# Performance work log

Measured on AMD Instinct MI355X. Metric: run time of the kernel, lower is better.

Reference implementation:

```python
import jax, jax.numpy as jnp
import numpy as np

N = 36          # number of independent LSTM streams (input_dim)
H = 256         # hidden units
G = 4 * H       # gate width (i, f, g, o)
SPEC = 6
OUT = 30
B, T = 32, 128


def setup_inputs() -> dict:
    key = jax.random.key(0)
    ks = jax.random.split(key, 18)
    s = 0.05
    d = {}
    d["x"] = jax.random.normal(ks[0], (B, T, N), dtype=jnp.float32)
    d["spec"] = jax.random.normal(ks[1], (B, SPEC), dtype=jnp.float32)
    # 36 stacked 2-layer LSTMs, batched along leading stream axis N.
    # Layer 1: input_size=1, so W_ih collapses to [N, G].
    d["Wih1"] = jax.random.normal(ks[2], (N, G), dtype=jnp.float32) * s
    d["Whh1"] = jax.random.normal(ks[3], (N, G, H), dtype=jnp.float32) * s
    d["bih1"] = jax.random.normal(ks[4], (N, G), dtype=jnp.float32) * s
    d["bhh1"] = jax.random.normal(ks[5], (N, G), dtype=jnp.float32) * s
    # Layer 2: input_size=H.
    d["Wih2"] = jax.random.normal(ks[6], (N, G, H), dtype=jnp.float32) * s
    d["Whh2"] = jax.random.normal(ks[7], (N, G, H), dtype=jnp.float32) * s
    d["bih2"] = jax.random.normal(ks[8], (N, G), dtype=jnp.float32) * s
    d["bhh2"] = jax.random.normal(ks[9], (N, G), dtype=jnp.float32) * s
    # spec_dense: Linear(6, H); stored as [in, out].
    d["Wspec"] = jax.random.normal(ks[10], (SPEC, H), dtype=jnp.float32) * s
    d["bspec"] = jax.random.normal(ks[11], (H,), dtype=jnp.float32) * s
    # predicter: Linear(H*(N+1), H) -> ReLU -> Linear(H, OUT); stored as [in, out].
    d["Wp1"] = jax.random.normal(ks[12], (H * (N + 1), H), dtype=jnp.float32) * s
    d["bp1"] = jax.random.normal(ks[13], (H,), dtype=jnp.float32) * s
    d["Wp2"] = jax.random.normal(ks[14], (H, OUT), dtype=jnp.float32) * s
    d["bp2"] = jax.random.normal(ks[15], (OUT,), dtype=jnp.float32) * s
    return d


def _lstm_cell(gates, c):
    # torch gate order: input, forget, cell(g), output
    i, f, g, o = jnp.split(gates, 4, axis=-1)
    c = jax.nn.sigmoid(f) * c + jax.nn.sigmoid(i) * jnp.tanh(g)
    h = jax.nn.sigmoid(o) * jnp.tanh(c)
    return h, c


def reference(x, spec, Wih1, Whh1, bih1, bhh1, Wih2, Whh2, bih2, bhh2,
              Wspec, bspec, Wp1, bp1, Wp2, bp2):
    b = x.shape[0]
    bg1 = bih1 + bhh1  # [N, G]
    bg2 = bih2 + bhh2

    def step(carry, x_t):
        # x_t: [B, N] scalar input per stream at this timestep
        h1, c1, h2, c2 = carry
        g1 = x_t[:, :, None] * Wih1[None] + jnp.einsum('bnh,ngh->bng', h1, Whh1) + bg1
        h1, c1 = _lstm_cell(g1, c1)
        g2 = (jnp.einsum('bnh,ngh->bng', h1, Wih2)
              + jnp.einsum('bnh,ngh->bng', h2, Whh2) + bg2)
        h2, c2 = _lstm_cell(g2, c2)
        return (h1, c1, h2, c2), None

    z = jnp.zeros((b, N, H), x.dtype)
    (h1, c1, h2, c2), _ = jax.lax.scan(step, (z, z, z, z), jnp.transpose(x, (1, 0, 2)))
    hidden_all = h2.reshape(b, N * H)          # concat of last-step top-layer h per stream
    hidden_spec = spec @ Wspec + bspec         # [B, H]
    feat = jnp.concatenate([hidden_all, hidden_spec], axis=1)  # [B, (N+1)*H]
    return jax.nn.relu(feat @ Wp1 + bp1) @ Wp2 + bp2
```

## Files before the change

### kernel.cpp

```cpp
#include <hip/hip_runtime.h>
#include <cstdint>
#include <cstddef>


constexpr int kN = 36, kH = 256, kG = 1024, kB = 32, kT = 128, kSpec = 6, kOut = 30;
constexpr int kHP = 264;
constexpr int kD1 = 16;

typedef __bf16 bf16;
typedef __bf16 bf16x8 __attribute__((ext_vector_type(8)));
typedef float f32x4 __attribute__((ext_vector_type(4)));
typedef unsigned long long u64;
typedef unsigned int u32;

__device__ __forceinline__ float rcpf(float v) { return __builtin_amdgcn_rcpf(v); }
__device__ __forceinline__ float sigm(float v) { return rcpf(1.f + __expf(-v)); }
__device__ __forceinline__ float tanh_f(float v) {
  return fmaf(-2.f, rcpf(1.f + __expf(2.f * v)), 1.f);
}
__device__ __forceinline__ unsigned short f2bf(float f) {
  bf16 b = (bf16)f;
  return __builtin_bit_cast(unsigned short, b);
}
__device__ __forceinline__ u64 pload(const u64* p) {
  return __hip_atomic_load(p, __ATOMIC_RELAXED, __HIP_MEMORY_SCOPE_AGENT);
}
__device__ __forceinline__ void pstore(u64* p, u64 v) {
  __hip_atomic_store(p, v, __ATOMIC_RELAXED, __HIP_MEMORY_SCOPE_AGENT);
}
__device__ __forceinline__ u32 pload32(const u32* p) {
  return __hip_atomic_load(p, __ATOMIC_RELAXED, __HIP_MEMORY_SCOPE_AGENT);
}
__device__ __forceinline__ void pstore32(u32* p, u32 v) {
  __hip_atomic_store(p, v, __ATOMIC_RELAXED, __HIP_MEMORY_SCOPE_AGENT);
}


__device__ __forceinline__ void issue16(const u64* __restrict__ base, int tid, u64* v) {
#pragma unroll
  for (int i = 0; i < 16; ++i) v[i] = pload(base + (size_t)i * 256 + tid);
}
__device__ __forceinline__ void finish16(const u64* __restrict__ base, u32 want,
                                         int tid, u64* v) {
  u32 got = 0;
  for (;;) {
#pragma unroll
    for (int i = 0; i < 16; ++i)
      if (!(got & (1u << i)) && (u32)(v[i] >> 32) == want) got |= 1u << i;
    if (got == 0xFFFFu) return;
#pragma unroll
    for (int i = 0; i < 16; ++i)
      if (!(got & (1u << i))) v[i] = pload(base + (size_t)i * 256 + tid);
  }
}
__device__ __forceinline__ void finish16_stage(const u64* __restrict__ base, u32 want,
                                               int tid, unsigned short (*hs)[kHP],
                                               u64* v) {
  u32 got = 0;
  for (;;) {
#pragma unroll
    for (int i = 0; i < 16; ++i) {
      if (!(got & (1u << i)) && (u32)(v[i] >> 32) == want) {
        got |= 1u << i;
        hs[i][tid] = (unsigned short)v[i];
        hs[i + 16][tid] = (unsigned short)(v[i] >> 16);
      }
    }
    if (got == 0xFFFFu) return;
#pragma unroll
    for (int i = 0; i < 16; ++i)
      if (!(got & (1u << i))) v[i] = pload(base + (size_t)i * 256 + tid);
  }
}
__device__ __forceinline__ void issue8h(const u64* __restrict__ base, int tid, int pc0,
                                        u64* v) {
  const int c = pc0 + (tid & 127), m0 = (tid >> 7) * 8;
#pragma unroll
  for (int i = 0; i < 8; ++i) v[i] = pload(base + (size_t)(m0 + i) * 256 + c);
}
__device__ __forceinline__ void finish8_stage(const u64* __restrict__ base, u32 want,
                                              int tid, int pc0,
                                              unsigned short (*hs)[kHP], u64* v) {
  const int c = pc0 + (tid & 127), m0 = (tid >> 7) * 8;
  u32 got = 0;
  for (;;) {
#pragma unroll
    for (int i = 0; i < 8; ++i) {
      if (!(got & (1u << i)) && (u32)(v[i] >> 32) == want) {
        got |= 1u << i;
        hs[m0 + i][c] = (unsigned short)v[i];
        hs[m0 + i + 16][c] = (unsigned short)(v[i] >> 16);
      }
    }
    if (got == 0xFFu) return;
#pragma unroll
    for (int i = 0; i < 8; ++i)
      if (!(got & (1u << i))) v[i] = pload(base + (size_t)(m0 + i) * 256 + c);
  }
}

__global__ __launch_bounds__(256) void k_convert(
    const float* __restrict__ wa, const float* __restrict__ wb, const float* __restrict__ wc,
    bf16* __restrict__ oa, bf16* __restrict__ ob, bf16* __restrict__ oc)
{
  const size_t total = (size_t)kN * 64 * 8 * 64;
  size_t gid = (size_t)blockIdx.x * 256 + threadIdx.x;
  if (gid >= total) return;
  const int lane = (int)(gid & 63);
  const int ks = (int)((gid >> 6) & 7);
  const int nt = (int)((gid >> 9) & 63);
  const int n = (int)(gid >> 15);
  const int g = nt * 16 + (lane & 15);
  const int k = ks * 32 + (lane >> 4) * 8;
  const size_t so = ((size_t)n * kG + g) * kH + k;

  const float4 a0 = *(const float4*)(wa + so), a1 = *(const float4*)(wa + so + 4);
  const float4 b0 = *(const float4*)(wb + so), b1 = *(const float4*)(wb + so + 4);
  const float4 c0 = *(const float4*)(wc + so), c1 = *(const float4*)(wc + so + 4);
  bf16x8 va, vb, vc;
  va[0]=(bf16)a0.x; va[1]=(bf16)a0.y; va[2]=(bf16)a0.z; va[3]=(bf16)a0.w;
  va[4]=(bf16)a1.x; va[5]=(bf16)a1.y; va[6]=(bf16)a1.z; va[7]=(bf16)a1.w;
  vb[0]=(bf16)b0.x; vb[1]=(bf16)b0.y; vb[2]=(bf16)b0.z; vb[3]=(bf16)b0.w;
  vb[4]=(bf16)b1.x; vb[5]=(bf16)b1.y; vb[6]=(bf16)b1.z; vb[7]=(bf16)b1.w;
  vc[0]=(bf16)c0.x; vc[1]=(bf16)c0.y; vc[2]=(bf16)c0.z; vc[3]=(bf16)c0.w;
  vc[4]=(bf16)c1.x; vc[5]=(bf16)c1.y; vc[6]=(bf16)c1.z; vc[7]=(bf16)c1.w;
  ((bf16x8*)oa)[gid] = va;
  ((bf16x8*)ob)[gid] = vb;
  ((bf16x8*)oc)[gid] = vc;
}

#define L1_MFMA_HALF(KS0)                                                            \
  _Pragma("unroll")                                                                  \
  for (int kk = 0; kk < 4; ++kk) {                                                   \
    const int ks = (KS0) + kk;                                                       \
    bf16x8 A0 = *(const bf16x8*)&hs1[l15][ks * 32 + l4 * 8];                         \
    bf16x8 A1 = *(const bf16x8*)&hs1[16 + l15][ks * 32 + l4 * 8];                    \
    _Pragma("unroll")                                                                \
    for (int jj = 0; jj < 2; ++jj)                                                   \
      _Pragma("unroll")                                                              \
      for (int gt = 0; gt < 4; ++gt) {                                               \
        acc[0][jj][gt] = __builtin_amdgcn_mfma_f32_16x16x32_bf16(                    \
            A0, W[jj][gt][ks], acc[0][jj][gt], 0, 0, 0);                             \
        acc[1][jj][gt] = __builtin_amdgcn_mfma_f32_16x16x32_bf16(                    \
            A1, W[jj][gt][ks], acc[1][jj][gt], 0, 0, 0);                             \
      }                                                                              \
  }

__global__ __launch_bounds__(256) __attribute__((amdgpu_waves_per_eu(1, 1)))
void k_lstm(
    const float* __restrict__ x, const float* __restrict__ Wih1,
    const float* __restrict__ bih1, const float* __restrict__ bhh1,
    const float* __restrict__ bih2, const float* __restrict__ bhh2,
    const bf16* __restrict__ pk1, const bf16* __restrict__ pk2i,
    const bf16* __restrict__ pk2h, float* __restrict__ h2_final,
    u64* __restrict__ h1r, u64* __restrict__ h2r, u32* __restrict__ prog)
{
  const int blk = blockIdx.x;
  const int tid = threadIdx.x, wv = tid >> 6, lane = tid & 63;
  const int l15 = lane & 15, l4 = lane >> 4;

  __shared__ alignas(16) unsigned short hs1[kB][kHP];

  if (blk < 72) {
    const int n = blk >> 1, j = blk & 1;
    __shared__ float xsh[kT][kB];
    for (int i = tid; i < kB * kT; i += 256) {
      int b = i >> 7, t = i & 127;
      xsh[t][b] = x[((size_t)b * kT + t) * kN + n];
    }
    bf16x8 W[2][4][8];
    {
      const bf16x8* base = (const bf16x8*)pk1 + (size_t)n * 32768;
#pragma unroll
      for (int jj = 0; jj < 2; ++jj)
#pragma unroll
        for (int gt = 0; gt < 4; ++gt)
#pragma unroll
          for (int ks = 0; ks < 8; ++ks)
            W[jj][gt][ks] = base[(size_t)(gt * 16 + j * 8 + wv * 2 + jj) * 512 + ks * 64 + lane];
    }
    float wih[2][4], bg[2][4];
#pragma unroll
    for (int jj = 0; jj < 2; ++jj)
#pragma unroll
      for (int gt = 0; gt < 4; ++gt) {
        int g = gt * 256 + j * 128 + wv * 32 + jj * 16 + l15;
        wih[jj][gt] = Wih1[n * kG + g];
        bg[jj][gt] = bih1[n * kG + g] + bhh1[n * kG + g];
      }
    float cst[2][2][4];
#pragma unroll
    for (int a = 0; a < 2; ++a)
#pragma unroll
      for (int b = 0; b < 2; ++b)
#pragma unroll
        for (int r = 0; r < 4; ++r) cst[a][b][r] = 0.f;

    u64* ringn = h1r + (size_t)n * kD1 * 4096;
    u32* pg = prog + n * 4;
    const int pc0 = (1 - j) * 128, myb = j * 128 + wv * 32;
    u64 pv[8];
    __syncthreads();

#pragma unroll 1
    for (int t = 0; t < kT; ++t) {
      if ((t & 7) == 0 && t) {
        if (tid == 0) {
          for (;;) {
            u32 m0 = pload32(&pg[0]), m1 = pload32(&pg[1]);
            u32 m2 = pload32(&pg[2]), m3 = pload32(&pg[3]);
            u32 mn = m0 < m1 ? m0 : m1;
            mn = mn < m2 ? mn : m2;
            mn = mn < m3 ? mn : m3;
            if ((int)mn + 8 >= t) break;
          }
        }
        __syncthreads();
      }
      f32x4 acc[2][2][4];
#pragma unroll
      for (int mt = 0; mt < 2; ++mt)
#pragma unroll
        for (int jj = 0; jj < 2; ++jj)
#pragma unroll
          for (int gt = 0; gt < 4; ++gt)
#pragma unroll
            for (int r = 0; r < 4; ++r)
              acc[mt][jj][gt][r] = xsh[t][mt * 16 + l4 * 4 + r] * wih[jj][gt] + bg[jj][gt];
      if (t > 0) {
        const u64* ps = ringn + (size_t)((t - 1) % kD1) * 4096;
        if (j == 0) { L1_MFMA_HALF(0) } else { L1_MFMA_HALF(4) }
        finish8_stage(ps, (u32)t, tid, pc0, hs1, pv);
        __syncthreads();
        if (j == 0) { L1_MFMA_HALF(4) } else { L1_MFMA_HALF(0) }
      }
      u64* pub = ringn + (size_t)(t % kD1) * 4096;
      const u64 tagw = ((u64)(u32)(t + 1)) << 32;
      float hv[2][2][4];
#pragma unroll
      for (int jj = 0; jj < 2; ++jj) {
#pragma unroll
        for (int mt = 0; mt < 2; ++mt)
#pragma unroll
          for (int r = 0; r < 4; ++r) {
            float cc = sigm(acc[mt][jj][1][r]) * cst[mt][jj][r]
                     + sigm(acc[mt][jj][0][r]) * tanh_f(acc[mt][jj][2][r]);
            cst[mt][jj][r] = cc;
            hv[mt][jj][r] = sigm(acc[mt][jj][3][r]) * tanh_f(cc);
          }
#pragma unroll
        for (int r = 0; r < 4; ++r) {
          int c = myb + jj * 16 + l15, m = l4 * 4 + r;
          pstore(&pub[(size_t)m * 256 + c],
                 tagw | ((u64)f2bf(hv[1][jj][r]) << 16) | f2bf(hv[0][jj][r]));
        }
      }
#pragma unroll
      for (int mt = 0; mt < 2; ++mt)
#pragma unroll
        for (int jj = 0; jj < 2; ++jj)
#pragma unroll
          for (int r = 0; r < 4; ++r)
            hs1[mt * 16 + l4 * 4 + r][myb + jj * 16 + l15] = f2bf(hv[mt][jj][r]);
      if (t + 1 < kT) issue8h(pub, tid, pc0, pv);
      __syncthreads();
    }
  } else {
    const int bb = blk - 72, n = bb >> 2, q = bb & 3;
    __shared__ alignas(16) unsigned short hs2[kB][kHP];

    bf16x8 Wi[4][8], Wh[4][8];
    {
      const bf16x8* bi = (const bf16x8*)pk2i + (size_t)n * 32768;
      const bf16x8* bh = (const bf16x8*)pk2h + (size_t)n * 32768;
#pragma unroll
      for (int gt = 0; gt < 4; ++gt)
#pragma unroll
        for (int ks = 0; ks < 8; ++ks) {
          size_t o = (size_t)(gt * 16 + q * 4 + wv) * 512 + ks * 64 + lane;
          Wi[gt][ks] = bi[o];
          Wh[gt][ks] = bh[o];
        }
    }
    const int col = q * 64 + wv * 16 + l15;
    float bg[4];
#pragma unroll
    for (int gt = 0; gt < 4; ++gt) {
      int g = gt * 256 + col;
      bg[gt] = bih2[n * kG + g] + bhh2[n * kG + g];
    }
    float cst[2][4];
#pragma unroll
    for (int mt = 0; mt < 2; ++mt)
#pragma unroll
      for (int r = 0; r < 4; ++r) cst[mt][r] = 0.f;

    u64* ringn = h1r + (size_t)n * kD1 * 4096;
    u64* h2n = h2r + (size_t)n * 2 * 4096;
    u32* pg = prog + n * 4 + q;
    __syncthreads();

    u64 v1[16], v2[16];
    issue16(ringn, tid, v1);
    finish16(ringn, 1u, tid, v1);

#pragma unroll 1
    for (int t = 0; t < kT; ++t) {
#pragma unroll
      for (int i = 0; i < 16; ++i) {
        hs1[i][tid] = (unsigned short)v1[i];
        hs1[i + 16][tid] = (unsigned short)(v1[i] >> 16);
      }
      __syncthreads();
      if (tid == 0) pstore32(pg, (u32)(t + 1));
      const u64* pn = ringn + (size_t)((t + 1) % kD1) * 4096;
      if (t + 1 < kT) issue16(pn, tid, v1);
      f32x4 acc[2][4];
#pragma unroll
      for (int mt = 0; mt < 2; ++mt)
#pragma unroll
        for (int gt = 0; gt < 4; ++gt)
#pragma unroll
          for (int r = 0; r < 4; ++r) acc[mt][gt][r] = bg[gt];
#pragma unroll
      for (int ks = 0; ks < 8; ++ks) {
        bf16x8 A0 = *(const bf16x8*)&hs1[l15][ks * 32 + l4 * 8];
        bf16x8 A1 = *(const bf16x8*)&hs1[16 + l15][ks * 32 + l4 * 8];
#pragma unroll
        for (int gt = 0; gt < 4; ++gt) {
          acc[0][gt] = __builtin_amdgcn_mfma_f32_16x16x32_bf16(A0, Wi[gt][ks], acc[0][gt], 0, 0, 0);
          acc[1][gt] = __builtin_amdgcn_mfma_f32_16x16x32_bf16(A1, Wi[gt][ks], acc[1][gt], 0, 0, 0);
        }
      }
      if (t > 0) {
        finish16_stage(h2n + (size_t)((t - 1) & 1) * 4096, (u32)t, tid, hs2, v2);
        __syncthreads();
#pragma unroll
        for (int ks = 0; ks < 8; ++ks) {
          bf16x8 A0 = *(const bf16x8*)&hs2[l15][ks * 32 + l4 * 8];
          bf16x8 A1 = *(const bf16x8*)&hs2[16 + l15][ks * 32 + l4 * 8];
#pragma unroll
          for (int gt = 0; gt < 4; ++gt) {
            acc[0][gt] = __builtin_amdgcn_mfma_f32_16x16x32_bf16(A0, Wh[gt][ks], acc[0][gt], 0, 0, 0);
            acc[1][gt] = __builtin_amdgcn_mfma_f32_16x16x32_bf16(A1, Wh[gt][ks], acc[1][gt], 0, 0, 0);
          }
        }
      }
      u64* pub = h2n + (size_t)(t & 1) * 4096;
      const u64 tagw = ((u64)(u32)(t + 1)) << 32;
      float hv[2][4];
#pragma unroll
      for (int r = 0; r < 4; ++r) {
#pragma unroll
        for (int mt = 0; mt < 2; ++mt) {
          float cc = sigm(acc[mt][1][r]) * cst[mt][r]
                   + sigm(acc[mt][0][r]) * tanh_f(acc[mt][2][r]);
          cst[mt][r] = cc;
          hv[mt][r] = sigm(acc[mt][3][r]) * tanh_f(cc);
        }
        pstore(&pub[(size_t)(l4 * 4 + r) * 256 + col],
               tagw | ((u64)f2bf(hv[1][r]) << 16) | f2bf(hv[0][r]));
      }
      if (t == kT - 1) {
#pragma unroll
        for (int mt = 0; mt < 2; ++mt)
#pragma unroll
          for (int r = 0; r < 4; ++r)
            h2_final[((size_t)n * kB + (mt * 16 + l4 * 4 + r)) * kH + col] = hv[mt][r];
      }
      if (t + 1 < kT) issue16(pub, tid, v2);
      if (t + 1 < kT) finish16(pn, (u32)(t + 2), tid, v1);
      __syncthreads();
    }
  }
}

__global__ __launch_bounds__(256) void k_head1(
    const float* __restrict__ spec, const float* __restrict__ Wspec,
    const float* __restrict__ bspec, const float* __restrict__ Wp1,
    const float* __restrict__ h2f, float* __restrict__ partial)
{
  const int kc = blockIdx.x;
  const int b = blockIdx.y;
  const int o = threadIdx.x;
  __shared__ float fs[kH];
  if (kc < kN) {
    fs[o] = h2f[((size_t)kc * kB + b) * kH + o];
  } else {
    float v = bspec[o];
#pragma unroll
    for (int s = 0; s < kSpec; ++s) v += spec[b * kSpec + s] * Wspec[s * kH + o];
    fs[o] = v;
  }
  __syncthreads();
  const float* __restrict__ wp = Wp1 + (size_t)kc * 256 * kH + o;
  float a = 0.f;
#pragma unroll 8
  for (int i = 0; i < 256; ++i) a += fs[i] * wp[(size_t)i * kH];
  partial[((size_t)kc * kB + b) * kH + o] = a;
}

__global__ __launch_bounds__(256) void k_head2(
    const float* __restrict__ bp1, const float* __restrict__ Wp2,
    const float* __restrict__ bp2, const float* __restrict__ partial,
    float* __restrict__ out)
{
  const int b = blockIdx.x;
  const int o = threadIdx.x;
  __shared__ float hid[kH];
  float a = bp1[o];
#pragma unroll
  for (int kc = 0; kc < kN + 1; ++kc) a += partial[((size_t)kc * kB + b) * kH + o];
  hid[o] = fmaxf(a, 0.f);
  __syncthreads();
  if (o < kOut) {
    float r = bp2[o];
#pragma unroll 8
    for (int h = 0; h < kH; ++h) r += hid[h] * Wp2[h * kOut + o];
    out[b * kOut + o] = r;
  }
}

extern "C" void kernel_launch(void* const* d_in, const int* in_sizes, int n_in,
                              void* d_out, int out_size, void* d_ws, size_t ws_size,
                              hipStream_t stream) {
  const float* x = (const float*)d_in[0];
  const float* spec = (const float*)d_in[1];
  const float* Wih1 = (const float*)d_in[2];
  const float* Whh1 = (const float*)d_in[3];
  const float* bih1 = (const float*)d_in[4];
  const float* bhh1 = (const float*)d_in[5];
  const float* Wih2 = (const float*)d_in[6];
  const float* Whh2 = (const float*)d_in[7];
  const float* bih2 = (const float*)d_in[8];
  const float* bhh2 = (const float*)d_in[9];
  const float* Wspec = (const float*)d_in[10];
  const float* bspec = (const float*)d_in[11];
  const float* Wp1 = (const float*)d_in[12];
  const float* bp1 = (const float*)d_in[13];
  const float* Wp2 = (const float*)d_in[14];
  const float* bp2 = (const float*)d_in[15];
  float* out = (float*)d_out;

  const size_t WSZ = (size_t)kN * kG * kH;
  u32* prog = (u32*)d_ws;
  u64* h1r = (u64*)((char*)d_ws + 4096);
  u64* h2r = h1r + (size_t)kN * kD1 * 4096;
  bf16* pk1 = (bf16*)(h2r + (size_t)kN * 2 * 4096);
  bf16* pk2i = pk1 + WSZ;
  bf16* pk2h = pk2i + WSZ;
  float* h2_final = (float*)(pk2h + WSZ);
  float* partial = h2_final + (size_t)kN * kB * kH;

  hipMemsetAsync(d_ws, 0, 4096, stream);

  const size_t groups = (size_t)kN * 64 * 8 * 64;
  k_convert<<<dim3((unsigned)((groups + 255) / 256)), dim3(256), 0, stream>>>(
      Whh1, Wih2, Whh2, pk1, pk2i, pk2h);
  k_lstm<<<dim3(216), dim3(256), 0, stream>>>(
      x, Wih1, bih1, bhh1, bih2, bhh2, pk1, pk2i, pk2h, h2_final, h1r, h2r, prog);
  k_head1<<<dim3(kN + 1, kB), dim3(256), 0, stream>>>(spec, Wspec, bspec, Wp1, h2_final, partial);
  k_head2<<<dim3(kB), dim3(256), 0, stream>>>(bp1, Wp2, bp2, partial, out);
}
```

Baseline: 879.2 us.

## Keep own h2 slice locally and rotate K order to overlap peer waits

Each layer-2 block now writes its own freshly computed h2 columns straight into shared memory and fetches only the other three quarter-slices from peers (12 loads instead of 16). The Whh2 K-chunks are rotated so the chunks this block owns locally are multiplied first, before it waits on peer data, hiding part of the cross-block handoff latency. Staging of the next h1 into shared memory is also moved to the end of the step, which removes one barrier per step. Correctness now depends on the rotated weight indexing and the column mapping (fm/fc) matching exactly, and the per-element index arrays add register pressure.

```diff
diff --git a/kernel.cpp b/kernel.cpp
--- a/kernel.cpp
+++ b/kernel.cpp
@@ -53,23 +53,28 @@
       if (!(got & (1u << i))) v[i] = pload(base + (size_t)i * 256 + tid);
   }
 }
-__device__ __forceinline__ void finish16_stage(const u64* __restrict__ base, u32 want,
-                                               int tid, unsigned short (*hs)[kHP],
-                                               u64* v) {
+__device__ __forceinline__ void issue12(const u64* __restrict__ base, const int* fm,
+                                        const int* fc, u64* v) {
+#pragma unroll
+  for (int i = 0; i < 12; ++i) v[i] = pload(base + (size_t)fm[i] * 256 + fc[i]);
+}
+__device__ __forceinline__ void finish12_stage(const u64* __restrict__ base, u32 want,
+                                               const int* fm, const int* fc,
+                                               unsigned short (*hs)[kHP], u64* v) {
   u32 got = 0;
   for (;;) {
 #pragma unroll
-    for (int i = 0; i < 16; ++i) {
+    for (int i = 0; i < 12; ++i) {
       if (!(got & (1u << i)) && (u32)(v[i] >> 32) == want) {
         got |= 1u << i;
-        hs[i][tid] = (unsigned short)v[i];
-        hs[i + 16][tid] = (unsigned short)(v[i] >> 16);
-      }
-    }
-    if (got == 0xFFFFu) return;
-#pragma unroll
-    for (int i = 0; i < 16; ++i)
-      if (!(got & (1u << i))) v[i] = pload(base + (size_t)i * 256 + tid);
+        hs[fm[i]][fc[i]] = (unsigned short)v[i];
+        hs[fm[i] + 16][fc[i]] = (unsigned short)(v[i] >> 16);
+      }
+    }
+    if (got == 0xFFFu) return;
+#pragma unroll
+    for (int i = 0; i < 12; ++i)
+      if (!(got & (1u << i))) v[i] = pload(base + (size_t)fm[i] * 256 + fc[i]);
   }
 }
 __device__ __forceinline__ void issue8h(const u64* __restrict__ base, int tid, int pc0,
@@ -276,11 +281,22 @@
 #pragma unroll
       for (int gt = 0; gt < 4; ++gt)
 #pragma unroll
-        for (int ks = 0; ks < 8; ++ks) {
-          size_t o = (size_t)(gt * 16 + q * 4 + wv) * 512 + ks * 64 + lane;
-          Wi[gt][ks] = bi[o];
-          Wh[gt][ks] = bh[o];
-        }
+        for (int i = 0; i < 8; ++i) {
+          size_t nt = (size_t)(gt * 16 + q * 4 + wv) * 512;
+          Wi[gt][i] = bi[nt + (size_t)i * 64 + lane];
+          Wh[gt][i] = bh[nt + (size_t)((2 * q + i) & 7) * 64 + lane];
+        }
+    }
+    int cb[8];
+#pragma unroll
+    for (int i = 0; i < 8; ++i) cb[i] = ((2 * q + i) & 7) * 32;
+    int fm[12], fc[12];
+#pragma unroll
+    for (int i = 0; i < 12; ++i) {
+      int p = tid * 12 + i;
+      int m = p / 192;
+      fm[i] = m;
+      fc[i] = (q * 64 + 64 + (p - m * 192)) & 255;
     }
     const int col = q * 64 + wv * 16 + l15;
     float bg[4];
@@ -300,18 +316,18 @@
     u32* pg = prog + n * 4 + q;
     __syncthreads();
 
-    u64 v1[16], v2[16];
+    u64 v1[16], v2[12];
     issue16(ringn, tid, v1);
     finish16(ringn, 1u, tid, v1);
+#pragma unroll
+    for (int i = 0; i < 16; ++i) {
+      hs1[i][tid] = (unsigned short)v1[i];
+      hs1[i + 16][tid] = (unsigned short)(v1[i] >> 16);
+    }
+    __syncthreads();
 
 #pragma unroll 1
     for (int t = 0; t < kT; ++t) {
-#pragma unroll
-      for (int i = 0; i < 16; ++i) {
-        hs1[i][tid] = (unsigned short)v1[i];
-        hs1[i + 16][tid] = (unsigned short)(v1[i] >> 16);
-      }
-      __syncthreads();
       if (tid == 0) pstore32(pg, (u32)(t + 1));
       const u64* pn = ringn + (size_t)((t + 1) % kD1) * 4096;
       if (t + 1 < kT) issue16(pn, tid, v1);
@@ -333,18 +349,30 @@
         }
       }
       if (t > 0) {
-        finish16_stage(h2n + (size_t)((t - 1) & 1) * 4096, (u32)t, tid, hs2, v2);
+#pragma unroll
+        for (int i = 0; i < 2; ++i) {
+          bf16x8 A0 = *(const bf16x8*)&hs2[l15][cb[i] + l4 * 8];
+          bf16x8 A1 = *(const bf16x8*)&hs2[16 + l15][cb[i] + l4 * 8];
+#pragma unroll
+          for (int gt = 0; gt < 4; ++gt) {
+            acc[0][gt] = __builtin_amdgcn_mfma_f32_16x16x32_bf16(A0, Wh[gt][i], acc[0][gt], 0, 0, 0);
+            acc[1][gt] = __builtin_amdgcn_mfma_f32_16x16x32_bf16(A1, Wh[gt][i], acc[1][gt], 0, 0, 0);
+          }
+        }
+        finish12_stage(h2n + (size_t)((t - 1) & 1) * 4096, (u32)t, fm, fc, hs2, v2);
         __syncthreads();
 #pragma unroll
-        for (int ks = 0; ks < 8; ++ks) {
-          bf16x8 A0 = *(const bf16x8*)&hs2[l15][ks * 32 + l4 * 8];
-          bf16x8 A1 = *(const bf16x8*)&hs2[16 + l15][ks * 32 + l4 * 8];
+        for (int i = 2; i < 8; ++i) {
+          bf16x8 A0 = *(const bf16x8*)&hs2[l15][cb[i] + l4 * 8];
+          bf16x8 A1 = *(const bf16x8*)&hs2[16 + l15][cb[i] + l4 * 8];
 #pragma unroll
           for (int gt = 0; gt < 4; ++gt) {
-            acc[0][gt] = __builtin_amdgcn_mfma_f32_16x16x32_bf16(A0, Wh[gt][ks], acc[0][gt], 0, 0, 0);
-            acc[1][gt] = __builtin_amdgcn_mfma_f32_16x16x32_bf16(A1, Wh[gt][ks], acc[1][gt], 0, 0, 0);
+            acc[0][gt] = __builtin_amdgcn_mfma_f32_16x16x32_bf16(A0, Wh[gt][i], acc[0][gt], 0, 0, 0);
+            acc[1][gt] = __builtin_amdgcn_mfma_f32_16x16x32_bf16(A1, Wh[gt][i], acc[1][gt], 0, 0, 0);
           }
         }
+      } else {
+        __syncthreads();
       }
       u64* pub = h2n + (size_t)(t & 1) * 4096;
       const u64 tagw = ((u64)(u32)(t + 1)) << 32;
@@ -360,6 +388,8 @@
         }
         pstore(&pub[(size_t)(l4 * 4 + r) * 256 + col],
                tagw | ((u64)f2bf(hv[1][r]) << 16) | f2bf(hv[0][r]));
+        hs2[l4 * 4 + r][col] = f2bf(hv[0][r]);
+        hs2[l4 * 4 + r + 16][col] = f2bf(hv[1][r]);
       }
       if (t == kT - 1) {
 #pragma unroll
@@ -368,8 +398,15 @@
           for (int r = 0; r < 4; ++r)
             h2_final[((size_t)n * kB + (mt * 16 + l4 * 4 + r)) * kH + col] = hv[mt][r];
       }
-      if (t + 1 < kT) issue16(pub, tid, v2);
-      if (t + 1 < kT) finish16(pn, (u32)(t + 2), tid, v1);
+      if (t + 1 < kT) issue12(pub, fm, fc, v2);
+      if (t + 1 < kT) {
+        finish16(pn, (u32)(t + 2), tid, v1);
+#pragma unroll
+        for (int i = 0; i < 16; ++i) {
+          hs1[i][tid] = (unsigned short)v1[i];
+          hs1[i + 16][tid] = (unsigned short)(v1[i] >> 16);
+        }
+      }
       __syncthreads();
     }
   }
```

Result: slower. 1.878 ms (+113.6%).

## Overlap layer-2 recurrent MFMA with peer h2 exchange via rotated K order

Applied to the files above, without the earlier changes.

Each layer-2 block now writes its own freshly computed h2 slice directly into local shared memory. It also rotates the K-chunk order of the recurrent weights so the first two chunks, its own columns, are multiplied before waiting on the other blocks' published h2. This overlaps part of the recurrent GEMM with the cross-block exchange latency. The risk is a race: the local hs2 writes happen before the barrier that finish16_stage and later reads rely on, so ordering against the staged copy must stay correct.

```diff
diff --git a/kernel.cpp b/kernel.cpp
--- a/kernel.cpp
+++ b/kernel.cpp
@@ -276,12 +276,15 @@
 #pragma unroll
       for (int gt = 0; gt < 4; ++gt)
 #pragma unroll
-        for (int ks = 0; ks < 8; ++ks) {
-          size_t o = (size_t)(gt * 16 + q * 4 + wv) * 512 + ks * 64 + lane;
-          Wi[gt][ks] = bi[o];
-          Wh[gt][ks] = bh[o];
-        }
-    }
+        for (int i = 0; i < 8; ++i) {
+          size_t nt = (size_t)(gt * 16 + q * 4 + wv) * 512;
+          Wi[gt][i] = bi[nt + (size_t)i * 64 + lane];
+          Wh[gt][i] = bh[nt + (size_t)((2 * q + i) & 7) * 64 + lane];
+        }
+    }
+    int cb[8];
+#pragma unroll
+    for (int i = 0; i < 8; ++i) cb[i] = ((2 * q + i) & 7) * 32;
     const int col = q * 64 + wv * 16 + l15;
     float bg[4];
 #pragma unroll
@@ -333,16 +336,26 @@
         }
       }
       if (t > 0) {
+#pragma unroll
+        for (int i = 0; i < 2; ++i) {
+          bf16x8 A0 = *(const bf16x8*)&hs2[l15][cb[i] + l4 * 8];
+          bf16x8 A1 = *(const bf16x8*)&hs2[16 + l15][cb[i] + l4 * 8];
+#pragma unroll
+          for (int gt = 0; gt < 4; ++gt) {
+            acc[0][gt] = __builtin_amdgcn_mfma_f32_16x16x32_bf16(A0, Wh[gt][i], acc[0][gt], 0, 0, 0);
+            acc[1][gt] = __builtin_amdgcn_mfma_f32_16x16x32_bf16(A1, Wh[gt][i], acc[1][gt], 0, 0, 0);
+          }
+        }
         finish16_stage(h2n + (size_t)((t - 1) & 1) * 4096, (u32)t, tid, hs2, v2);
         __syncthreads();
 #pragma unroll
-        for (int ks = 0; ks < 8; ++ks) {
-          bf16x8 A0 = *(const bf16x8*)&hs2[l15][ks * 32 + l4 * 8];
-          bf16x8 A1 = *(const bf16x8*)&hs2[16 + l15][ks * 32 + l4 * 8];
+        for (int i = 2; i < 8; ++i) {
+          bf16x8 A0 = *(const bf16x8*)&hs2[l15][cb[i] + l4 * 8];
+          bf16x8 A1 = *(const bf16x8*)&hs2[16 + l15][cb[i] + l4 * 8];
 #pragma unroll
           for (int gt = 0; gt < 4; ++gt) {
-            acc[0][gt] = __builtin_amdgcn_mfma_f32_16x16x32_bf16(A0, Wh[gt][ks], acc[0][gt], 0, 0, 0);
-            acc[1][gt] = __builtin_amdgcn_mfma_f32_16x16x32_bf16(A1, Wh[gt][ks], acc[1][gt], 0, 0, 0);
+            acc[0][gt] = __builtin_amdgcn_mfma_f32_16x16x32_bf16(A0, Wh[gt][i], acc[0][gt], 0, 0, 0);
+            acc[1][gt] = __builtin_amdgcn_mfma_f32_16x16x32_bf16(A1, Wh[gt][i], acc[1][gt], 0, 0, 0);
           }
         }
       }
@@ -360,6 +373,8 @@
         }
         pstore(&pub[(size_t)(l4 * 4 + r) * 256 + col],
                tagw | ((u64)f2bf(hv[1][r]) << 16) | f2bf(hv[0][r]));
+        hs2[l4 * 4 + r][col] = f2bf(hv[0][r]);
+        hs2[l4 * 4 + r + 16][col] = f2bf(hv[1][r]);
       }
       if (t == kT - 1) {
 #pragma unroll
```

New measurement: 1.005 ms. 1.14x slower.

## Colocate each stream's blocks on one XCD and add fast-path h exchange

Applied to the files above, without the earlier changes.

Blocks are remapped so that all six workgroups of a stream (two layer-1, four layer-2) land on the same XCD, assuming round-robin dispatch by block index. Each producer also writes its tagged hidden-state packets to a second double-buffered array with ordinary stores. Consumers first poll that array with batched sc0 inline-asm loads, which the XCD-local L2 may serve without the system-coherent path, and fall back to the original polling after repeated misses. The goal is lower cross-block handoff latency per timestep, at the cost of extra stores, a larger workspace, 24 idle blocks, and reliance on the dispatch-order assumption and on sc0 coherence semantics.

```diff
diff --git a/kernel.cpp b/kernel.cpp
--- a/kernel.cpp
+++ b/kernel.cpp
@@ -97,6 +97,78 @@
     for (int i = 0; i < 8; ++i)
       if (!(got & (1u << i))) v[i] = pload(base + (size_t)(m0 + i) * 256 + c);
   }
+}
+
+__device__ __forceinline__ void fast_load16(const u64* fb, int tid, u64* v) {
+  const u64* b0 = fb + 2 * 256 + tid;
+  const u64* b1 = fb + 6 * 256 + tid;
+  const u64* b2 = fb + 10 * 256 + tid;
+  const u64* b3 = fb + 14 * 256 + tid;
+  asm volatile(
+      "global_load_dwordx2 %0, %16, off offset:-4096 sc0\n\t"
+      "global_load_dwordx2 %1, %16, off offset:-2048 sc0\n\t"
+      "global_load_dwordx2 %2, %16, off sc0\n\t"
+      "global_load_dwordx2 %3, %16, off offset:2048 sc0\n\t"
+      "global_load_dwordx2 %4, %17, off offset:-4096 sc0\n\t"
+      "global_load_dwordx2 %5, %17, off offset:-2048 sc0\n\t"
+      "global_load_dwordx2 %6, %17, off sc0\n\t"
+      "global_load_dwordx2 %7, %17, off offset:2048 sc0\n\t"
+      "global_load_dwordx2 %8, %18, off offset:-4096 sc0\n\t"
+      "global_load_dwordx2 %9, %18, off offset:-2048 sc0\n\t"
+      "global_load_dwordx2 %10, %18, off sc0\n\t"
+      "global_load_dwordx2 %11, %18, off offset:2048 sc0\n\t"
+      "global_load_dwordx2 %12, %19, off offset:-4096 sc0\n\t"
+      "global_load_dwordx2 %13, %19, off offset:-2048 sc0\n\t"
+      "global_load_dwordx2 %14, %19, off sc0\n\t"
+      "global_load_dwordx2 %15, %19, off offset:2048 sc0\n\t"
+      "s_waitcnt vmcnt(0)"
+      : "=v"(v[0]), "=v"(v[1]), "=v"(v[2]), "=v"(v[3]),
+        "=v"(v[4]), "=v"(v[5]), "=v"(v[6]), "=v"(v[7]),
+        "=v"(v[8]), "=v"(v[9]), "=v"(v[10]), "=v"(v[11]),
+        "=v"(v[12]), "=v"(v[13]), "=v"(v[14]), "=v"(v[15])
+      : "v"(b0), "v"(b1), "v"(b2), "v"(b3)
+      : "memory");
+}
+__device__ __forceinline__ bool fast_try16(const u64* fb, u32 want, int tid, u64* v,
+                                           int budget) {
+  for (int it = 0; it < budget; ++it) {
+    fast_load16(fb, tid, v);
+    bool all = true;
+#pragma unroll
+    for (int i = 0; i < 16; ++i) all &= ((u32)(v[i] >> 32) == want);
+    if (all) return true;
+  }
+  return false;
+}
+__device__ __forceinline__ void fast_load8(const u64* fb, int tid, int pc0, u64* v) {
+  const int c = pc0 + (tid & 127), m0 = (tid >> 7) * 8;
+  const u64* b0 = fb + (size_t)(m0 + 2) * 256 + c;
+  const u64* b1 = fb + (size_t)(m0 + 6) * 256 + c;
+  asm volatile(
+      "global_load_dwordx2 %0, %8, off offset:-4096 sc0\n\t"
+      "global_load_dwordx2 %1, %8, off offset:-2048 sc0\n\t"
+      "global_load_dwordx2 %2, %8, off sc0\n\t"
+      "global_load_dwordx2 %3, %8, off offset:2048 sc0\n\t"
+      "global_load_dwordx2 %4, %9, off offset:-4096 sc0\n\t"
+      "global_load_dwordx2 %5, %9, off offset:-2048 sc0\n\t"
+      "global_load_dwordx2 %6, %9, off sc0\n\t"
+      "global_load_dwordx2 %7, %9, off offset:2048 sc0\n\t"
+      "s_waitcnt vmcnt(0)"
+      : "=v"(v[0]), "=v"(v[1]), "=v"(v[2]), "=v"(v[3]),
+        "=v"(v[4]), "=v"(v[5]), "=v"(v[6]), "=v"(v[7])
+      : "v"(b0), "v"(b1)
+      : "memory");
+}
+__device__ __forceinline__ bool fast_try8(const u64* fb, u32 want, int tid, int pc0,
+                                          u64* v, int budget) {
+  for (int it = 0; it < budget; ++it) {
+    fast_load8(fb, tid, pc0, v);
+    bool all = true;
+#pragma unroll
+    for (int i = 0; i < 8; ++i) all &= ((u32)(v[i] >> 32) == want);
+    if (all) return true;
+  }
+  return false;
 }
 
 __global__ __launch_bounds__(256) void k_convert(
@@ -153,16 +225,21 @@
     const float* __restrict__ bih2, const float* __restrict__ bhh2,
     const bf16* __restrict__ pk1, const bf16* __restrict__ pk2i,
     const bf16* __restrict__ pk2h, float* __restrict__ h2_final,
-    u64* __restrict__ h1r, u64* __restrict__ h2r, u32* __restrict__ prog)
+    u64* __restrict__ h1r, u64* __restrict__ h2r,
+    u64* __restrict__ fh1, u64* __restrict__ fh2, u32* __restrict__ prog)
 {
   const int blk = blockIdx.x;
+  const int xcd = blk & 7, sl = blk >> 3;
+  const int kk_ = sl / 6, w = sl - kk_ * 6;
+  const int n = kk_ * 8 + xcd;
+  if (n >= kN) return;
   const int tid = threadIdx.x, wv = tid >> 6, lane = tid & 63;
   const int l15 = lane & 15, l4 = lane >> 4;
 
   __shared__ alignas(16) unsigned short hs1[kB][kHP];
 
-  if (blk < 72) {
-    const int n = blk >> 1, j = blk & 1;
+  if (w < 2) {
+    const int j = w;
     __shared__ float xsh[kT][kB];
     for (int i = tid; i < kB * kT; i += 256) {
       int b = i >> 7, t = i & 127;
@@ -197,9 +274,11 @@
         for (int r = 0; r < 4; ++r) cst[a][b][r] = 0.f;
 
     u64* ringn = h1r + (size_t)n * kD1 * 4096;
+    u64* fh1n = fh1 + (size_t)n * 2 * 4096;
     u32* pg = prog + n * 4;
     const int pc0 = (1 - j) * 128, myb = j * 128 + wv * 32;
-    u64 pv[8];
+    u64 pv[8], vf[8];
+    int fen = 1, fmiss = 0;
     __syncthreads();
 
 #pragma unroll 1
@@ -230,11 +309,25 @@
       if (t > 0) {
         const u64* ps = ringn + (size_t)((t - 1) % kD1) * 4096;
         if (j == 0) { L1_MFMA_HALF(0) } else { L1_MFMA_HALF(4) }
-        finish8_stage(ps, (u32)t, tid, pc0, hs1, pv);
+        bool fok = false;
+        if (fen) fok = fast_try8(fh1n + (size_t)((t - 1) & 1) * 4096, (u32)t, tid, pc0, vf, 12);
+        if (fok) {
+          const int c = pc0 + (tid & 127), m0 = (tid >> 7) * 8;
+          fmiss = 0;
+#pragma unroll
+          for (int i = 0; i < 8; ++i) {
+            hs1[m0 + i][c] = (unsigned short)vf[i];
+            hs1[m0 + i + 16][c] = (unsigned short)(vf[i] >> 16);
+          }
+        } else {
+          if (fen && ++fmiss >= 4) fen = 0;
+          finish8_stage(ps, (u32)t, tid, pc0, hs1, pv);
+        }
         __syncthreads();
         if (j == 0) { L1_MFMA_HALF(4) } else { L1_MFMA_HALF(0) }
       }
       u64* pub = ringn + (size_t)(t % kD1) * 4096;
+      u64* fpub = fh1n + (size_t)(t & 1) * 4096;
       const u64 tagw = ((u64)(u32)(t + 1)) << 32;
       float hv[2][2][4];
 #pragma unroll
@@ -251,8 +344,9 @@
 #pragma unroll
         for (int r = 0; r < 4; ++r) {
           int c = myb + jj * 16 + l15, m = l4 * 4 + r;
-          pstore(&pub[(size_t)m * 256 + c],
-                 tagw | ((u64)f2bf(hv[1][jj][r]) << 16) | f2bf(hv[0][jj][r]));
+          u64 pkt = tagw | ((u64)f2bf(hv[1][jj][r]) << 16) | f2bf(hv[0][jj][r]);
+          fpub[(size_t)m * 256 + c] = pkt;
+          pstore(&pub[(size_t)m * 256 + c], pkt);
         }
       }
 #pragma unroll
@@ -266,7 +360,7 @@
       __syncthreads();
     }
   } else {
-    const int bb = blk - 72, n = bb >> 2, q = bb & 3;
+    const int q = w - 2;
     __shared__ alignas(16) unsigned short hs2[kB][kHP];
 
     bf16x8 Wi[4][8], Wh[4][8];
@@ -297,10 +391,12 @@
 
     u64* ringn = h1r + (size_t)n * kD1 * 4096;
     u64* h2n = h2r + (size_t)n * 2 * 4096;
+    u64* fh2n = fh2 + (size_t)n * 2 * 4096;
     u32* pg = prog + n * 4 + q;
+    int fen = 1, fmiss = 0;
     __syncthreads();
 
-    u64 v1[16], v2[16];
+    u64 v1[16], v2[16], vf[16];
     issue16(ringn, tid, v1);
     finish16(ringn, 1u, tid, v1);
 
@@ -333,7 +429,19 @@
         }
       }
       if (t > 0) {
-        finish16_stage(h2n + (size_t)((t - 1) & 1) * 4096, (u32)t, tid, hs2, v2);
+        bool fok = false;
+        if (fen) fok = fast_try16(fh2n + (size_t)((t - 1) & 1) * 4096, (u32)t, tid, vf, 12);
+        if (fok) {
+          fmiss = 0;
+#pragma unroll
+          for (int i = 0; i < 16; ++i) {
+            hs2[i][tid] = (unsigned short)vf[i];
+            hs2[i + 16][tid] = (unsigned short)(vf[i] >> 16);
+          }
+        } else {
+          if (fen && ++fmiss >= 4) fen = 0;
+          finish16_stage(h2n + (size_t)((t - 1) & 1) * 4096, (u32)t, tid, hs2, v2);
+        }
         __syncthreads();
 #pragma unroll
         for (int ks = 0; ks < 8; ++ks) {
@@ -347,6 +455,7 @@
         }
       }
       u64* pub = h2n + (size_t)(t & 1) * 4096;
+      u64* fpub = fh2n + (size_t)(t & 1) * 4096;
       const u64 tagw = ((u64)(u32)(t + 1)) << 32;
       float hv[2][4];
 #pragma unroll
@@ -358,8 +467,9 @@
           cst[mt][r] = cc;
           hv[mt][r] = sigm(acc[mt][3][r]) * tanh_f(cc);
         }
-        pstore(&pub[(size_t)(l4 * 4 + r) * 256 + col],
-               tagw | ((u64)f2bf(hv[1][r]) << 16) | f2bf(hv[0][r]));
+        u64 pkt = tagw | ((u64)f2bf(hv[1][r]) << 16) | f2bf(hv[0][r]);
+        fpub[(size_t)(l4 * 4 + r) * 256 + col] = pkt;
+        pstore(&pub[(size_t)(l4 * 4 + r) * 256 + col], pkt);
       }
       if (t == kT - 1) {
 #pragma unroll
@@ -446,7 +556,9 @@
   u32* prog = (u32*)d_ws;
   u64* h1r = (u64*)((char*)d_ws + 4096);
   u64* h2r = h1r + (size_t)kN * kD1 * 4096;
-  bf16* pk1 = (bf16*)(h2r + (size_t)kN * 2 * 4096);
+  u64* fh1 = h2r + (size_t)kN * 2 * 4096;
+  u64* fh2 = fh1 + (size_t)kN * 2 * 4096;
+  bf16* pk1 = (bf16*)(fh2 + (size_t)kN * 2 * 4096);
   bf16* pk2i = pk1 + WSZ;
   bf16* pk2h = pk2i + WSZ;
   float* h2_final = (float*)(pk2h + WSZ);
@@ -457,8 +569,9 @@
   const size_t groups = (size_t)kN * 64 * 8 * 64;
   k_convert<<<dim3((unsigned)((groups + 255) / 256)), dim3(256), 0, stream>>>(
       Whh1, Wih2, Whh2, pk1, pk2i, pk2h);
-  k_lstm<<<dim3(216), dim3(256), 0, stream>>>(
-      x, Wih1, bih1, bhh1, bih2, bhh2, pk1, pk2i, pk2h, h2_final, h1r, h2r, prog);
+  k_lstm<<<dim3(240), dim3(256), 0, stream>>>(
+      x, Wih1, bih1, bhh1, bih2, bhh2, pk1, pk2i, pk2h, h2_final,
+      h1r, h2r, fh1, fh2, prog);
   k_head1<<<dim3(kN + 1, kB), dim3(256), 0, stream>>>(spec, Wspec, bspec, Wp1, h2_final, partial);
   k_head2<<<dim3(kB), dim3(256), 0, stream>>>(bp1, Wp2, bp2, partial, out);
 }
```

New measurement: 964.5 us. 1.1x slower.
